# Kernel optimization log

Measured on AMD Instinct MI355X. Metric: run time of the kernel, lower is better.

## Reference

```python
import jax, jax.numpy as jnp
import numpy as np

B, N, F, H, K = 4, 512, 64, 64, 64
EPS = 1e-14


def _pair_proj(h, W):
    # Linear over concat([h_j, h_i]) == h_j @ W[:F] + h_i @ W[F:], broadcast to [B,N,N,out]
    f = h.shape[-1]
    pj = h @ W[:f]   # [B,N,out] contribution of h.unsqueeze(-3) (index j)
    pi = h @ W[f:]   # [B,N,out] contribution of h.unsqueeze(-2) (index i)
    return pj[:, None, :, :] + pi[:, :, None, :]


def setup_inputs() -> dict:
    key = jax.random.key(0)
    ks = jax.random.split(key, 10)
    def w(k, shape, fan_in):
        return (jax.random.normal(k, shape, dtype=jnp.float32) / np.float32(np.sqrt(fan_in)))
    return {
        "h": jax.random.normal(ks[0], (B, N, F), dtype=jnp.float32),
        "x": jax.random.normal(ks[1], (B, N, 3), dtype=jnp.float32),
        "W_ew": w(ks[2], (2 * F, K), 2 * F), "b_ew": jnp.zeros((K,), jnp.float32),
        "W_sa": w(ks[3], (2 * F, 1), 2 * F),
        "W_es": w(ks[4], (2 * F + 1, H), 2 * F + 1), "b_es": jnp.zeros((H,), jnp.float32),
        "W_c1": w(ks[5], (H, H), H), "b_c1": jnp.zeros((H,), jnp.float32),
        "W_c2": w(ks[6], (H, 1), H), "b_c2": jnp.zeros((1,), jnp.float32),
        "W_n": w(ks[7], (F + H + K, H), F + H + K), "b_n": jnp.zeros((H,), jnp.float32),
    }


def reference(h, x, W_ew, b_ew, W_sa, W_es, b_es, W_c1, b_c1, W_c2, b_c2, W_n, b_n):
    # x_minus_xt[b,i,j] = x[b,j] - x[b,i]    [B,N,N,3]
    xmx = x[:, None, :, :] - x[:, :, None, :]
    norm = jnp.sqrt(jax.nn.relu(jnp.sum(xmx * xmx, axis=-1, keepdims=True)) + EPS)  # [B,N,N,1]
    spatial_att = jax.nn.softmax(norm, axis=-2)                                    # softmax over j
    filtered = 1.0 / (norm + 0.1)                                                  # [B,N,N,1]

    # edge_weight_mlp: tanh(Linear(2F -> K)) over h_cat_ht, without materializing the concat
    ew = jnp.tanh(_pair_proj(h, W_ew) + b_ew)                                      # [B,N,N,K]
    # semantic_attention_mlp: LeakyReLU(Linear(2F -> 1, no bias))
    sem_att = jax.nn.leaky_relu(_pair_proj(h, W_sa), negative_slope=0.01)          # [B,N,N,1]

    # x_minus_xt_att_sum = sum_j ew[b,i,j,k] * (xmx / norm^2)[b,i,j,c] -> [B,N,K,3]
    v = xmx / (norm * norm + EPS)
    att_sum = jnp.einsum('bijk,bijc->bikc', ew, v)
    att_norm = jnp.sqrt(jax.nn.relu(jnp.sum(att_sum * att_sum, axis=-1)) + EPS)    # [B,N,K]

    # edge_summary_mlp: SiLU(Linear(cat([filtered, h_j, h_i]) -> H))
    pre = filtered * W_es[0] + _pair_proj(h, W_es[1:]) + b_es                      # [B,N,N,H]
    h_e = jax.nn.silu(pre)

    # coordinate update: Linear->SiLU->Linear(H->1)
    coord = jax.nn.silu(h_e @ W_c1 + b_c1) @ W_c2 + b_c2                           # [B,N,N,1]
    x_new = jnp.sum(xmx * coord, axis=-2) + x                                      # sum over j

    h_e_agg = jnp.sum(sem_att * spatial_att * h_e, axis=-2)                        # [B,N,H]
    h_new = jnp.concatenate([h, h_e_agg, att_norm], axis=-1) @ W_n + b_n           # [B,N,H]
    return h_new, x_new
```

## Files before the change

kernel.cpp:

```cpp
#include <hip/hip_runtime.h>

#define B_ 4
#define N_ 512
#define F_ 64
#define H_ 64
#define K_ 64
#define BN_ (B_*N_)
#define EPS_ 1e-14f
#define TSC 2.8853900817779268f

typedef __attribute__((ext_vector_type(8))) short short8;
typedef __attribute__((ext_vector_type(4))) float f32x4;
typedef __attribute__((ext_vector_type(2))) float f32x2;

__device__ __forceinline__ unsigned short f2bf(float f) {
    const unsigned u = __float_as_uint(f);
    return (unsigned short)((u + 0x7FFFu + ((u >> 16) & 1u)) >> 16);
}
__device__ __forceinline__ unsigned short cvt_bf16(float f) {
    unsigned r;
    asm("v_cvt_pk_bf16_f32 %0, %1, %1" : "=v"(r) : "v"(f));
    return (unsigned short)r;
}
__device__ __forceinline__ unsigned cvt_pk_bf16(float lo, float hi) {
    unsigned r;
    asm("v_cvt_pk_bf16_f32 %0, %1, %2" : "=v"(r) : "v"(lo), "v"(hi));
    return r;
}
__device__ __forceinline__ float exp2_raw(float x) {
    float r;
    asm("v_exp_f32 %0, %1" : "=v"(r) : "v"(x));
    return r;
}
__device__ __forceinline__ float lane_bcast(float v, int lane) {
    return __int_as_float(__builtin_amdgcn_readlane(__float_as_int(v), lane));
}
__device__ __forceinline__ float rcpf(float x) { return __builtin_amdgcn_rcpf(x); }
__device__ __forceinline__ float fast_silu(float x) {
    return x * rcpf(1.0f + __expf(-x));
}

#define W_PJ2  0
#define W_PIEW (BN_*128)
#define W_PIES (BN_*128 + BN_*64)
#define W_PJSA (BN_*128 + 2*BN_*64)
#define W_PISA (BN_*128 + 2*BN_*64 + BN_)

__global__ __launch_bounds__(256) void proj_kernel(
    const float* __restrict__ h, const float* __restrict__ W_ew,
    const float* __restrict__ W_sa, const float* __restrict__ W_es,
    float* __restrict__ ws)
{
    const int tid  = threadIdx.x;
    const int w    = tid >> 6;
    const int lane = tid & 63;
    const int node0 = blockIdx.x * 8;

    __shared__ float sW_ew[128][64];
    __shared__ float sW_es[128][64];
    __shared__ float sW_sa[128];
    __shared__ float sh[8][64];

    #pragma unroll
    for (int it = 0; it < 32; ++it) {
        const int idx = it*256 + tid;
        sW_ew[idx>>6][idx&63] = W_ew[idx];
        sW_es[idx>>6][idx&63] = W_es[64 + idx];
    }
    if (tid < 128) sW_sa[tid] = W_sa[tid];
    #pragma unroll
    for (int it = 0; it < 2; ++it) {
        const int idx = it*256 + tid;
        sh[idx>>6][idx&63] = h[node0*F_ + idx];
    }
    __syncthreads();

    const int n0 = w*2;
    float jew0=0.f,iew0=0.f,jes0=0.f,ies0=0.f;
    float jew1=0.f,iew1=0.f,jes1=0.f,ies1=0.f;
    #pragma unroll 8
    for (int f = 0; f < 64; ++f) {
        const float wje = sW_ew[f][lane],    wie = sW_ew[64+f][lane];
        const float wjs = sW_es[f][lane],    wis = sW_es[64+f][lane];
        const float h0  = sh[n0][f],         h1  = sh[n0+1][f];
        jew0 = fmaf(h0, wje, jew0);  iew0 = fmaf(h0, wie, iew0);
        jes0 = fmaf(h0, wjs, jes0);  ies0 = fmaf(h0, wis, ies0);
        jew1 = fmaf(h1, wje, jew1);  iew1 = fmaf(h1, wie, iew1);
        jes1 = fmaf(h1, wjs, jes1);  ies1 = fmaf(h1, wis, ies1);
    }
    float p0 = sh[n0][lane]   * sW_sa[lane];
    float q0 = sh[n0][lane]   * sW_sa[64+lane];
    float p1 = sh[n0+1][lane] * sW_sa[lane];
    float q1 = sh[n0+1][lane] * sW_sa[64+lane];
    #pragma unroll
    for (int m = 32; m >= 1; m >>= 1) {
        p0 += __shfl_xor(p0, m, 64);  q0 += __shfl_xor(q0, m, 64);
        p1 += __shfl_xor(p1, m, 64);  q1 += __shfl_xor(q1, m, 64);
    }

    const int g0 = node0 + n0;
    const int g1 = g0 + 1;
    ws[W_PJ2 + (size_t)g0*128 + lane*2 + 0] = jew0 * TSC;
    ws[W_PJ2 + (size_t)g0*128 + lane*2 + 1] = jes0;
    ws[W_PJ2 + (size_t)g1*128 + lane*2 + 0] = jew1 * TSC;
    ws[W_PJ2 + (size_t)g1*128 + lane*2 + 1] = jes1;
    ws[W_PIEW + g0*K_ + lane] = iew0;
    ws[W_PIEW + g1*K_ + lane] = iew1;
    ws[W_PIES + g0*H_ + lane] = ies0;
    ws[W_PIES + g1*H_ + lane] = ies1;
    if (lane == 0) {
        ws[W_PJSA + g0] = p0;  ws[W_PISA + g0] = q0;
        ws[W_PJSA + g1] = p1;  ws[W_PISA + g1] = q1;
    }
}

__global__ __launch_bounds__(256, 5) void main_kernel(
    const float* __restrict__ h, const float* __restrict__ x,
    const float* __restrict__ b_ew, const float* __restrict__ b_es,
    const float* __restrict__ W_es, const float* __restrict__ W_c1,
    const float* __restrict__ b_c1, const float* __restrict__ W_c2,
    const float* __restrict__ b_c2, const float* __restrict__ W_n,
    const float* __restrict__ b_n,
    const float* __restrict__ ws, float* __restrict__ out)
{
    const int bi   = blockIdx.x;
    const int b    = bi >> 9;
    const int base = b * N_;
    const int tid  = threadIdx.x;
    const int w    = tid >> 6;
    const int lane = tid & 63;
    const int quad = lane >> 4;
    const int l16  = lane & 15;

    __shared__ unsigned short he_buf[4][16][72];
    __shared__ float sdA[4][64][4];
    __shared__ float coord_buf[4][64];
    __shared__ unsigned short WT[64*64];
    __shared__ float s_bw[64][2];

    float* const epi = (float*)&he_buf[0][0][0];
#define S_ATT(cmp, wv, ln) epi[(cmp)*256 + (wv)*64 + (ln)]
#define S_HEA(wv, ln)      epi[768 + (wv)*64 + (ln)]
#define S_MISC(wv, k)      epi[1024 + (wv)*4 + (k)]
#define S_CONCAT(m)        epi[1040 + (m)]
#define S_HNEW(wv, ln)     epi[1240 + (wv)*64 + (ln)]

    {
        const int col = tid & 63;
        const int k0  = (tid >> 6) * 16;
        const unsigned swz = (col & 7) << 4;
        #pragma unroll
        for (int m = 0; m < 8; ++m) {
            const int k = k0 + 2*m;
            const float f0 = W_c1[k*H_ + col];
            const float f1 = W_c1[(k+1)*H_ + col];
            *(unsigned*)((char*)WT + (col*128 + ((2*k) ^ swz))) = cvt_pk_bf16(f0, f1);
        }
        if (tid < 64) { s_bw[tid][0] = b_c1[tid]; s_bw[tid][1] = W_c2[tid]; }
    }

    const float pi_ew_t = (ws[W_PIEW + bi*K_ + lane] + b_ew[lane]) * TSC;
    const float pi_es_t = ws[W_PIES + bi*H_ + lane] + b_es[lane];
    const float pisa    = ws[W_PISA + bi];
    const float xi0 = x[bi*3+0], xi1 = x[bi*3+1], xi2 = x[bi*3+2];
    const float wes0_t = W_es[lane];
    const float bc2    = b_c2[0];

    const unsigned swzl = (l16 & 7) << 4;
    const unsigned offB0 = (unsigned)l16*128 + (((unsigned)quad*16) ^ swzl);
    const unsigned offB1 = (unsigned)l16*128 + ((64u + (unsigned)quad*16) ^ swzl);

    __syncthreads();

    float att0=0.f, att1=0.f, att2=0.f, hea=0.f, sume=0.f;
    float xa0=0.f, xa1=0.f, xa2=0.f;

    for (int c = 0; c < 2; ++c) {
        const int j0 = (w*2 + c) * 64;

        float esem, d0, d1, d2;
        {
            const int gj = base + j0 + lane;
            d0 = x[gj*3+0] - xi0;
            d1 = x[gj*3+1] - xi1;
            d2 = x[gj*3+2] - xi2;
            const float d2s = fmaf(d0,d0, fmaf(d1,d1, d2*d2));
            const float nrm = sqrtf(d2s + EPS_);
            const float e   = __expf(nrm);
            sume += e;
            const float filt = rcpf(nrm + 0.1f);
            const float inv  = rcpf(fmaf(nrm, nrm, EPS_));
            const float sv   = ws[W_PJSA + gj] + pisa;
            const float sem  = (sv >= 0.f) ? sv : 0.01f*sv;
            esem = e * sem;
            f32x4 p0 = { d0*inv, d1*inv, d2*inv, filt };
            *(f32x4*)&sdA[w][lane][0] = p0;
        }

        #pragma unroll
        for (int s = 0; s < 4; ++s) {
            const int sj = s*16;
            const float* pjp = ws + W_PJ2 + (size_t)(base + j0 + sj)*128 + lane*2;
            #pragma unroll 4
            for (int jj = 0; jj < 16; ++jj) {
                const f32x2 pj = *(const f32x2*)(pjp + (size_t)jj*128);
                const f32x4 p0 = *(const f32x4*)&sdA[w][sj + jj][0];
                const float esem_s = lane_bcast(esem, sj + jj);
                const float pre = fmaf(p0.w, wes0_t, pj.y + pi_es_t);
                const float he  = fast_silu(pre);
                hea = fmaf(esem_s, he, hea);
                he_buf[w][jj][lane] = cvt_bf16(he);
                const float ewt = fmaf(-2.0f, rcpf(exp2_raw(pj.x + pi_ew_t) + 1.0f), 1.0f);
                att0 = fmaf(ewt, p0.x, att0);
                att1 = fmaf(ewt, p0.y, att1);
                att2 = fmaf(ewt, p0.z, att2);
            }

            {
                const short8 a0 = *(const short8*)&he_buf[w][l16][quad*8];
                const short8 a1 = *(const short8*)&he_buf[w][l16][32 + quad*8];
                float rs0=0.f, rs1=0.f, rs2=0.f, rs3=0.f;
                #pragma unroll
                for (int nt = 0; nt < 4; ++nt) {
                    const short8 b0 = *(const short8*)((const char*)WT + (nt*2048 + offB0));
                    const short8 b1 = *(const short8*)((const char*)WT + (nt*2048 + offB1));
                    const f32x2 bw = *(const f32x2*)&s_bw[nt*16 + l16][0];
                    f32x4 acc = {0.f, 0.f, 0.f, 0.f};
                    acc = __builtin_amdgcn_mfma_f32_16x16x32_bf16(a0, b0, acc, 0, 0, 0);
                    acc = __builtin_amdgcn_mfma_f32_16x16x32_bf16(a1, b1, acc, 0, 0, 0);
                    rs0 += fast_silu(acc[0] + bw.x) * bw.y;
                    rs1 += fast_silu(acc[1] + bw.x) * bw.y;
                    rs2 += fast_silu(acc[2] + bw.x) * bw.y;
                    rs3 += fast_silu(acc[3] + bw.x) * bw.y;
                }
                #pragma unroll
                for (int m = 1; m <= 8; m <<= 1) {
                    rs0 += __shfl_xor(rs0, m, 64);
                    rs1 += __shfl_xor(rs1, m, 64);
                    rs2 += __shfl_xor(rs2, m, 64);
                    rs3 += __shfl_xor(rs3, m, 64);
                }
                if (l16 == 0) {
                    f32x4 cv = { rs0 + bc2, rs1 + bc2, rs2 + bc2, rs3 + bc2 };
                    *(f32x4*)&coord_buf[w][sj + quad*4] = cv;
                }
            }
        }

        {
            const float cj = coord_buf[w][lane];
            xa0 = fmaf(d0, cj, xa0);
            xa1 = fmaf(d1, cj, xa1);
            xa2 = fmaf(d2, cj, xa2);
        }
    }

    __syncthreads();

    #pragma unroll
    for (int m = 32; m >= 1; m >>= 1) {
        sume += __shfl_xor(sume, m, 64);
        xa0  += __shfl_xor(xa0,  m, 64);
        xa1  += __shfl_xor(xa1,  m, 64);
        xa2  += __shfl_xor(xa2,  m, 64);
    }
    S_ATT(0, w, lane) = att0;
    S_ATT(1, w, lane) = att1;
    S_ATT(2, w, lane) = att2;
    S_HEA(w, lane)    = hea;
    if (lane == 0) {
        S_MISC(w, 0) = sume; S_MISC(w, 1) = xa0; S_MISC(w, 2) = xa1; S_MISC(w, 3) = xa2;
    }
    __syncthreads();

    if (w == 0) {
        const float a0 = S_ATT(0,0,lane)+S_ATT(0,1,lane)+S_ATT(0,2,lane)+S_ATT(0,3,lane);
        const float a1 = S_ATT(1,0,lane)+S_ATT(1,1,lane)+S_ATT(1,2,lane)+S_ATT(1,3,lane);
        const float a2 = S_ATT(2,0,lane)+S_ATT(2,1,lane)+S_ATT(2,2,lane)+S_ATT(2,3,lane);
        const float hg = S_HEA(0,lane)+S_HEA(1,lane)+S_HEA(2,lane)+S_HEA(3,lane);
        const float se = S_MISC(0,0)+S_MISC(1,0)+S_MISC(2,0)+S_MISC(3,0);
        const float attn = sqrtf(fmaf(a0,a0, fmaf(a1,a1, a2*a2)) + EPS_);
        S_CONCAT(lane)       = h[bi*F_ + lane];
        S_CONCAT(64 + lane)  = hg * rcpf(se);
        S_CONCAT(128 + lane) = attn;
    }
    if (tid < 3) {
        const float xat = S_MISC(0,1+tid)+S_MISC(1,1+tid)+S_MISC(2,1+tid)+S_MISC(3,1+tid);
        out[(size_t)BN_*H_ + bi*3 + tid] = x[bi*3+tid] + xat;
    }
    __syncthreads();

    {
        float acc = 0.f;
        const int m0 = w * 48;
        #pragma unroll 8
        for (int m = m0; m < m0 + 48; ++m)
            acc = fmaf(S_CONCAT(m), W_n[m*H_ + lane], acc);
        S_HNEW(w, lane) = acc;
    }
    __syncthreads();
    if (w == 0) {
        out[bi*H_ + lane] = S_HNEW(0,lane) + S_HNEW(1,lane)
                          + S_HNEW(2,lane) + S_HNEW(3,lane) + b_n[lane];
    }
}

extern "C" void kernel_launch(void* const* d_in, const int* in_sizes, int n_in,
                              void* d_out, int out_size, void* d_ws, size_t ws_size,
                              hipStream_t stream) {
    (void)in_sizes; (void)n_in; (void)out_size; (void)ws_size;
    const float* h    = (const float*)d_in[0];
    const float* x    = (const float*)d_in[1];
    const float* W_ew = (const float*)d_in[2];
    const float* b_ew = (const float*)d_in[3];
    const float* W_sa = (const float*)d_in[4];
    const float* W_es = (const float*)d_in[5];
    const float* b_es = (const float*)d_in[6];
    const float* W_c1 = (const float*)d_in[7];
    const float* b_c1 = (const float*)d_in[8];
    const float* W_c2 = (const float*)d_in[9];
    const float* b_c2 = (const float*)d_in[10];
    const float* W_n  = (const float*)d_in[11];
    const float* b_n  = (const float*)d_in[12];
    float* out = (float*)d_out;
    float* ws  = (float*)d_ws;

    proj_kernel<<<dim3(BN_/8), dim3(256), 0, stream>>>(h, W_ew, W_sa, W_es, ws);
    main_kernel<<<dim3(BN_), dim3(256), 0, stream>>>(h, x, b_ew, b_es, W_es, W_c1,
                                                     b_c1, W_c2, b_c2, W_n, b_n, ws, out);
}
```

Measured before the change: 156.6 us.

## Process two query nodes per block to reuse j-side projection loads

Each block now handles two consecutive i-nodes instead of one, so every load of the j-side projections (pj, x_j, pjsa) and every W_c1 staging into LDS serves two rows. The grid is halved and launch bounds drop to 4 waves per SIMD to make room for the doubled register state and LDS buffers. The aim is to cut global/L2 traffic on the per-j projection stream and amortise per-block setup. In exchange, register pressure and LDS use go up, occupancy drops, and the grid shrinks to 1024 blocks.

```diff
diff --git a/kernel.cpp b/kernel.cpp
--- a/kernel.cpp
+++ b/kernel.cpp
@@ -13,10 +13,6 @@
 typedef __attribute__((ext_vector_type(4))) float f32x4;
 typedef __attribute__((ext_vector_type(2))) float f32x2;
 
-__device__ __forceinline__ unsigned short f2bf(float f) {
-    const unsigned u = __float_as_uint(f);
-    return (unsigned short)((u + 0x7FFFu + ((u >> 16) & 1u)) >> 16);
-}
 __device__ __forceinline__ unsigned short cvt_bf16(float f) {
     unsigned r;
     asm("v_cvt_pk_bf16_f32 %0, %1, %1" : "=v"(r) : "v"(f));
@@ -114,7 +110,7 @@
     }
 }
 
-__global__ __launch_bounds__(256, 5) void main_kernel(
+__global__ __launch_bounds__(256, 4) void main_kernel(
     const float* __restrict__ h, const float* __restrict__ x,
     const float* __restrict__ b_ew, const float* __restrict__ b_es,
     const float* __restrict__ W_es, const float* __restrict__ W_c1,
@@ -123,8 +119,9 @@
     const float* __restrict__ b_n,
     const float* __restrict__ ws, float* __restrict__ out)
 {
-    const int bi   = blockIdx.x;
-    const int b    = bi >> 9;
+    const int bi0  = blockIdx.x * 2;
+    const int bi1  = bi0 + 1;
+    const int b    = bi0 >> 9;
     const int base = b * N_;
     const int tid  = threadIdx.x;
     const int w    = tid >> 6;
@@ -132,18 +129,18 @@
     const int quad = lane >> 4;
     const int l16  = lane & 15;
 
-    __shared__ unsigned short he_buf[4][16][72];
-    __shared__ float sdA[4][64][4];
-    __shared__ float coord_buf[4][64];
+    __shared__ unsigned short he_buf[2][4][16][72];
+    __shared__ float sdA[2][4][64][4];
+    __shared__ float coord_buf[2][4][64];
     __shared__ unsigned short WT[64*64];
     __shared__ float s_bw[64][2];
 
-    float* const epi = (float*)&he_buf[0][0][0];
-#define S_ATT(cmp, wv, ln) epi[(cmp)*256 + (wv)*64 + (ln)]
-#define S_HEA(wv, ln)      epi[768 + (wv)*64 + (ln)]
-#define S_MISC(wv, k)      epi[1024 + (wv)*4 + (k)]
-#define S_CONCAT(m)        epi[1040 + (m)]
-#define S_HNEW(wv, ln)     epi[1240 + (wv)*64 + (ln)]
+    float* const epi = (float*)&he_buf[0][0][0][0];
+#define S_ATT(ii,cmp,wv,ln) epi[(ii)*768 + (cmp)*256 + (wv)*64 + (ln)]
+#define S_HEA(ii,wv,ln)     epi[1536 + (ii)*256 + (wv)*64 + (ln)]
+#define S_MISC(ii,wv,k)     epi[2048 + (ii)*16 + (wv)*4 + (k)]
+#define S_CONCAT(ii,m)      epi[2080 + (ii)*192 + (m)]
+#define S_HNEW(ii,hf,ln)    epi[2464 + (ii)*128 + (hf)*64 + (ln)]
 
     {
         const int col = tid & 63;
@@ -159,10 +156,14 @@
         if (tid < 64) { s_bw[tid][0] = b_c1[tid]; s_bw[tid][1] = W_c2[tid]; }
     }
 
-    const float pi_ew_t = (ws[W_PIEW + bi*K_ + lane] + b_ew[lane]) * TSC;
-    const float pi_es_t = ws[W_PIES + bi*H_ + lane] + b_es[lane];
-    const float pisa    = ws[W_PISA + bi];
-    const float xi0 = x[bi*3+0], xi1 = x[bi*3+1], xi2 = x[bi*3+2];
+    const float pi_ew0 = (ws[W_PIEW + bi0*K_ + lane] + b_ew[lane]) * TSC;
+    const float pi_ew1 = (ws[W_PIEW + bi1*K_ + lane] + b_ew[lane]) * TSC;
+    const float pi_es0 = ws[W_PIES + bi0*H_ + lane] + b_es[lane];
+    const float pi_es1 = ws[W_PIES + bi1*H_ + lane] + b_es[lane];
+    const float pisa0  = ws[W_PISA + bi0];
+    const float pisa1  = ws[W_PISA + bi1];
+    const float xi00 = x[bi0*3+0], xi01 = x[bi0*3+1], xi02 = x[bi0*3+2];
+    const float xi10 = x[bi1*3+0], xi11 = x[bi1*3+1], xi12 = x[bi1*3+2];
     const float wes0_t = W_es[lane];
     const float bc2    = b_c2[0];
 
@@ -172,53 +173,86 @@
 
     __syncthreads();
 
-    float att0=0.f, att1=0.f, att2=0.f, hea=0.f, sume=0.f;
-    float xa0=0.f, xa1=0.f, xa2=0.f;
+    float att00=0.f, att01=0.f, att02=0.f, hea0=0.f, sume0=0.f;
+    float att10=0.f, att11=0.f, att12=0.f, hea1=0.f, sume1=0.f;
+    float xa00=0.f, xa01=0.f, xa02=0.f;
+    float xa10=0.f, xa11=0.f, xa12=0.f;
 
     for (int c = 0; c < 2; ++c) {
         const int j0 = (w*2 + c) * 64;
 
-        float esem, d0, d1, d2;
+        float esem0, esem1;
         {
             const int gj = base + j0 + lane;
-            d0 = x[gj*3+0] - xi0;
-            d1 = x[gj*3+1] - xi1;
-            d2 = x[gj*3+2] - xi2;
-            const float d2s = fmaf(d0,d0, fmaf(d1,d1, d2*d2));
-            const float nrm = sqrtf(d2s + EPS_);
-            const float e   = __expf(nrm);
-            sume += e;
-            const float filt = rcpf(nrm + 0.1f);
-            const float inv  = rcpf(fmaf(nrm, nrm, EPS_));
-            const float sv   = ws[W_PJSA + gj] + pisa;
-            const float sem  = (sv >= 0.f) ? sv : 0.01f*sv;
-            esem = e * sem;
-            f32x4 p0 = { d0*inv, d1*inv, d2*inv, filt };
-            *(f32x4*)&sdA[w][lane][0] = p0;
+            const float xj0 = x[gj*3+0], xj1 = x[gj*3+1], xj2 = x[gj*3+2];
+            const float pjsa = ws[W_PJSA + gj];
+            {
+                const float d0 = xj0-xi00, d1 = xj1-xi01, d2 = xj2-xi02;
+                const float d2s = fmaf(d0,d0, fmaf(d1,d1, d2*d2));
+                const float nrm = sqrtf(d2s + EPS_);
+                const float e   = __expf(nrm);
+                sume0 += e;
+                const float filt = rcpf(nrm + 0.1f);
+                const float inv  = rcpf(fmaf(nrm, nrm, EPS_));
+                const float sv   = pjsa + pisa0;
+                const float sem  = (sv >= 0.f) ? sv : 0.01f*sv;
+                esem0 = e * sem;
+                f32x4 p = { d0*inv, d1*inv, d2*inv, filt };
+                *(f32x4*)&sdA[0][w][lane][0] = p;
+            }
+            {
+                const float d0 = xj0-xi10, d1 = xj1-xi11, d2 = xj2-xi12;
+                const float d2s = fmaf(d0,d0, fmaf(d1,d1, d2*d2));
+                const float nrm = sqrtf(d2s + EPS_);
+                const float e   = __expf(nrm);
+                sume1 += e;
+                const float filt = rcpf(nrm + 0.1f);
+                const float inv  = rcpf(fmaf(nrm, nrm, EPS_));
+                const float sv   = pjsa + pisa1;
+                const float sem  = (sv >= 0.f) ? sv : 0.01f*sv;
+                esem1 = e * sem;
+                f32x4 p = { d0*inv, d1*inv, d2*inv, filt };
+                *(f32x4*)&sdA[1][w][lane][0] = p;
+            }
         }
 
         #pragma unroll
         for (int s = 0; s < 4; ++s) {
             const int sj = s*16;
             const float* pjp = ws + W_PJ2 + (size_t)(base + j0 + sj)*128 + lane*2;
-            #pragma unroll 4
+            #pragma unroll 2
             for (int jj = 0; jj < 16; ++jj) {
                 const f32x2 pj = *(const f32x2*)(pjp + (size_t)jj*128);
-                const f32x4 p0 = *(const f32x4*)&sdA[w][sj + jj][0];
-                const float esem_s = lane_bcast(esem, sj + jj);
-                const float pre = fmaf(p0.w, wes0_t, pj.y + pi_es_t);
-                const float he  = fast_silu(pre);
-                hea = fmaf(esem_s, he, hea);
-                he_buf[w][jj][lane] = cvt_bf16(he);
-                const float ewt = fmaf(-2.0f, rcpf(exp2_raw(pj.x + pi_ew_t) + 1.0f), 1.0f);
-                att0 = fmaf(ewt, p0.x, att0);
-                att1 = fmaf(ewt, p0.y, att1);
-                att2 = fmaf(ewt, p0.z, att2);
+                const f32x4 p0 = *(const f32x4*)&sdA[0][w][sj + jj][0];
+                const f32x4 p1 = *(const f32x4*)&sdA[1][w][sj + jj][0];
+                const float es0 = lane_bcast(esem0, sj + jj);
+                const float es1 = lane_bcast(esem1, sj + jj);
+                {
+                    const float pre = fmaf(p0.w, wes0_t, pj.y + pi_es0);
+                    const float he  = fast_silu(pre);
+                    hea0 = fmaf(es0, he, hea0);
+                    he_buf[0][w][jj][lane] = cvt_bf16(he);
+                    const float ewt = fmaf(-2.0f, rcpf(exp2_raw(pj.x + pi_ew0) + 1.0f), 1.0f);
+                    att00 = fmaf(ewt, p0.x, att00);
+                    att01 = fmaf(ewt, p0.y, att01);
+                    att02 = fmaf(ewt, p0.z, att02);
+                }
+                {
+                    const float pre = fmaf(p1.w, wes0_t, pj.y + pi_es1);
+                    const float he  = fast_silu(pre);
+                    hea1 = fmaf(es1, he, hea1);
+                    he_buf[1][w][jj][lane] = cvt_bf16(he);
+                    const float ewt = fmaf(-2.0f, rcpf(exp2_raw(pj.x + pi_ew1) + 1.0f), 1.0f);
+                    att10 = fmaf(ewt, p1.x, att10);
+                    att11 = fmaf(ewt, p1.y, att11);
+                    att12 = fmaf(ewt, p1.z, att12);
+                }
             }
 
-            {
-                const short8 a0 = *(const short8*)&he_buf[w][l16][quad*8];
-                const short8 a1 = *(const short8*)&he_buf[w][l16][32 + quad*8];
+            #pragma unroll
+            for (int ii = 0; ii < 2; ++ii) {
+                const short8 a0 = *(const short8*)&he_buf[ii][w][l16][quad*8];
+                const short8 a1 = *(const short8*)&he_buf[ii][w][l16][32 + quad*8];
                 float rs0=0.f, rs1=0.f, rs2=0.f, rs3=0.f;
                 #pragma unroll
                 for (int nt = 0; nt < 4; ++nt) {
@@ -242,16 +276,22 @@
                 }
                 if (l16 == 0) {
                     f32x4 cv = { rs0 + bc2, rs1 + bc2, rs2 + bc2, rs3 + bc2 };
-                    *(f32x4*)&coord_buf[w][sj + quad*4] = cv;
+                    *(f32x4*)&coord_buf[ii][w][sj + quad*4] = cv;
                 }
             }
         }
 
         {
-            const float cj = coord_buf[w][lane];
-            xa0 = fmaf(d0, cj, xa0);
-            xa1 = fmaf(d1, cj, xa1);
-            xa2 = fmaf(d2, cj, xa2);
+            const int gj = base + j0 + lane;
+            const float xj0 = x[gj*3+0], xj1 = x[gj*3+1], xj2 = x[gj*3+2];
+            const float cj0 = coord_buf[0][w][lane];
+            const float cj1 = coord_buf[1][w][lane];
+            xa00 = fmaf(xj0-xi00, cj0, xa00);
+            xa01 = fmaf(xj1-xi01, cj0, xa01);
+            xa02 = fmaf(xj2-xi02, cj0, xa02);
+            xa10 = fmaf(xj0-xi10, cj1, xa10);
+            xa11 = fmaf(xj1-xi11, cj1, xa11);
+            xa12 = fmaf(xj2-xi12, cj1, xa12);
         }
     }
 
@@ -259,49 +299,55 @@
 
     #pragma unroll
     for (int m = 32; m >= 1; m >>= 1) {
-        sume += __shfl_xor(sume, m, 64);
-        xa0  += __shfl_xor(xa0,  m, 64);
-        xa1  += __shfl_xor(xa1,  m, 64);
-        xa2  += __shfl_xor(xa2,  m, 64);
-    }
-    S_ATT(0, w, lane) = att0;
-    S_ATT(1, w, lane) = att1;
-    S_ATT(2, w, lane) = att2;
-    S_HEA(w, lane)    = hea;
+        sume0 += __shfl_xor(sume0, m, 64);
+        xa00  += __shfl_xor(xa00,  m, 64);
+        xa01  += __shfl_xor(xa01,  m, 64);
+        xa02  += __shfl_xor(xa02,  m, 64);
+        sume1 += __shfl_xor(sume1, m, 64);
+        xa10  += __shfl_xor(xa10,  m, 64);
+        xa11  += __shfl_xor(xa11,  m, 64);
+        xa12  += __shfl_xor(xa12,  m, 64);
+    }
+    S_ATT(0,0,w,lane) = att00;  S_ATT(0,1,w,lane) = att01;  S_ATT(0,2,w,lane) = att02;
+    S_ATT(1,0,w,lane) = att10;  S_ATT(1,1,w,lane) = att11;  S_ATT(1,2,w,lane) = att12;
+    S_HEA(0,w,lane) = hea0;     S_HEA(1,w,lane) = hea1;
     if (lane == 0) {
-        S_MISC(w, 0) = sume; S_MISC(w, 1) = xa0; S_MISC(w, 2) = xa1; S_MISC(w, 3) = xa2;
-    }
-    __syncthreads();
-
-    if (w == 0) {
-        const float a0 = S_ATT(0,0,lane)+S_ATT(0,1,lane)+S_ATT(0,2,lane)+S_ATT(0,3,lane);
-        const float a1 = S_ATT(1,0,lane)+S_ATT(1,1,lane)+S_ATT(1,2,lane)+S_ATT(1,3,lane);
-        const float a2 = S_ATT(2,0,lane)+S_ATT(2,1,lane)+S_ATT(2,2,lane)+S_ATT(2,3,lane);
-        const float hg = S_HEA(0,lane)+S_HEA(1,lane)+S_HEA(2,lane)+S_HEA(3,lane);
-        const float se = S_MISC(0,0)+S_MISC(1,0)+S_MISC(2,0)+S_MISC(3,0);
+        S_MISC(0,w,0) = sume0; S_MISC(0,w,1) = xa00; S_MISC(0,w,2) = xa01; S_MISC(0,w,3) = xa02;
+        S_MISC(1,w,0) = sume1; S_MISC(1,w,1) = xa10; S_MISC(1,w,2) = xa11; S_MISC(1,w,3) = xa12;
+    }
+    __syncthreads();
+
+    if ((w & 1) == 0) {
+        const int ii = w >> 1;
+        const int biX = bi0 + ii;
+        const float a0 = S_ATT(ii,0,0,lane)+S_ATT(ii,0,1,lane)+S_ATT(ii,0,2,lane)+S_ATT(ii,0,3,lane);
+        const float a1 = S_ATT(ii,1,0,lane)+S_ATT(ii,1,1,lane)+S_ATT(ii,1,2,lane)+S_ATT(ii,1,3,lane);
+        const float a2 = S_ATT(ii,2,0,lane)+S_ATT(ii,2,1,lane)+S_ATT(ii,2,2,lane)+S_ATT(ii,2,3,lane);
+        const float hg = S_HEA(ii,0,lane)+S_HEA(ii,1,lane)+S_HEA(ii,2,lane)+S_HEA(ii,3,lane);
+        const float se = S_MISC(ii,0,0)+S_MISC(ii,1,0)+S_MISC(ii,2,0)+S_MISC(ii,3,0);
         const float attn = sqrtf(fmaf(a0,a0, fmaf(a1,a1, a2*a2)) + EPS_);
-        S_CONCAT(lane)       = h[bi*F_ + lane];
-        S_CONCAT(64 + lane)  = hg * rcpf(se);
-        S_CONCAT(128 + lane) = attn;
-    }
-    if (tid < 3) {
-        const float xat = S_MISC(0,1+tid)+S_MISC(1,1+tid)+S_MISC(2,1+tid)+S_MISC(3,1+tid);
-        out[(size_t)BN_*H_ + bi*3 + tid] = x[bi*3+tid] + xat;
+        S_CONCAT(ii, lane)       = h[biX*F_ + lane];
+        S_CONCAT(ii, 64 + lane)  = hg * rcpf(se);
+        S_CONCAT(ii, 128 + lane) = attn;
+        if (lane < 3) {
+            const float xat = S_MISC(ii,0,1+lane)+S_MISC(ii,1,1+lane)+S_MISC(ii,2,1+lane)+S_MISC(ii,3,1+lane);
+            out[(size_t)BN_*H_ + biX*3 + lane] = x[biX*3+lane] + xat;
+        }
     }
     __syncthreads();
 
     {
+        const int ii = w >> 1, hf = w & 1;
         float acc = 0.f;
-        const int m0 = w * 48;
+        const int m0 = hf * 96;
         #pragma unroll 8
-        for (int m = m0; m < m0 + 48; ++m)
-            acc = fmaf(S_CONCAT(m), W_n[m*H_ + lane], acc);
-        S_HNEW(w, lane) = acc;
-    }
-    __syncthreads();
-    if (w == 0) {
-        out[bi*H_ + lane] = S_HNEW(0,lane) + S_HNEW(1,lane)
-                          + S_HNEW(2,lane) + S_HNEW(3,lane) + b_n[lane];
+        for (int m = m0; m < m0 + 96; ++m)
+            acc = fmaf(S_CONCAT(ii, m), W_n[m*H_ + lane], acc);
+        S_HNEW(ii, hf, lane) = acc;
+    }
+    __syncthreads();
+    if (w < 2) {
+        out[(bi0 + w)*H_ + lane] = S_HNEW(w,0,lane) + S_HNEW(w,1,lane) + b_n[lane];
     }
 }
 
@@ -326,6 +372,6 @@
     float* ws  = (float*)d_ws;
 
     proj_kernel<<<dim3(BN_/8), dim3(256), 0, stream>>>(h, W_ew, W_sa, W_es, ws);
-    main_kernel<<<dim3(BN_), dim3(256), 0, stream>>>(h, x, b_ew, b_es, W_es, W_c1,
-                                                     b_c1, W_c2, b_c2, W_n, b_n, ws, out);
-}
+    main_kernel<<<dim3(BN_/2), dim3(256), 0, stream>>>(h, x, b_ew, b_es, W_es, W_c1,
+                                                       b_c1, W_c2, b_c2, W_n, b_n, ws, out);
+}
```

After: 162.6 us. 1.04x slower.
